# Kernel tuning notes

Hardware: AMD Instinct MI355X
Metric: run time of the kernel (lower is better)

The kernel has to match this reference:

```python
import jax, jax.numpy as jnp
import numpy as np

BS, SEQ, NUM_SKILLS, DIM_S, SIZE_M = 64, 200, 4096, 256, 64

def setup_inputs():
    key = jax.random.key(0)
    ks = jax.random.split(key, 16)
    def n(k, shape, s=0.05):
        return jax.random.normal(k, shape, dtype=jnp.float32) * s
    return {
        "q": jax.random.randint(ks[0], (BS, SEQ), 0, NUM_SKILLS),
        "r": jax.random.randint(ks[1], (BS, SEQ), 0, 2),
        "k_emb": n(ks[2], (NUM_SKILLS, DIM_S)),
        "x_emb": n(ks[3], (2 * NUM_SKILLS + 1, DIM_S)),
        "Mk": n(ks[4], (SIZE_M, DIM_S)),
        "Mv0": n(ks[5], (SIZE_M, DIM_S)),
        "W_a": n(ks[6], (DIM_S, 2 * DIM_S)), "b_a": jnp.zeros((DIM_S,), jnp.float32),
        "W_e": n(ks[7], (DIM_S, DIM_S)), "b_e": jnp.zeros((DIM_S,), jnp.float32),
        "W_add": n(ks[8], (DIM_S, DIM_S)), "b_add": jnp.zeros((DIM_S,), jnp.float32),
        "W_f": n(ks[9], (DIM_S, 2 * DIM_S)), "b_f": jnp.zeros((DIM_S,), jnp.float32),
        "hx": n(ks[10], (1, DIM_S)), "cx": n(ks[11], (1, DIM_S)),
        "W_ih": n(ks[12], (4 * DIM_S, DIM_S)), "b_ih": jnp.zeros((4 * DIM_S,), jnp.float32),
        "W_hh": n(ks[13], (4 * DIM_S, DIM_S)), "b_hh": jnp.zeros((4 * DIM_S,), jnp.float32),
        "W_p": n(ks[14], (1, DIM_S)), "b_p": jnp.zeros((1,), jnp.float32),
    }

def _forward(q, r, k_emb, x_emb, Mk, Mv0, W_a, b_a, W_e, b_e, W_add, b_add,
             W_f, b_f, hx, cx, W_ih, b_ih, W_hh, b_hh, W_p, b_p):
    num_skills = k_emb.shape[0]
    bs = q.shape[0]
    k = k_emb[q]                                    # (bs, seq, d) question key embedding
    v = x_emb[q + num_skills * r]                   # (bs, seq, d) interaction embedding
    # DKVMN addressing against the static key memory Mk (precomputable for all t)
    w = jax.nn.softmax(jnp.einsum('bsd,md->bsm', k, Mk), axis=-1)
    # write control input: a_embed(cat(k, v)), then erase/add head projections
    we = jnp.einsum('bse,de->bsd', jnp.concatenate([k, v], axis=-1), W_a) + b_a
    erase = jax.nn.sigmoid(jnp.einsum('bsd,ed->bse', we, W_e) + b_e)
    add = jnp.tanh(jnp.einsum('bsd,ed->bse', we, W_add) + b_add)
    mem0 = jnp.broadcast_to(Mv0, (bs,) + Mv0.shape)  # (bs, m, d)

    def mem_step(mem, inp):
        wt, et, at = inp                             # (bs,m), (bs,d), (bs,d)
        read = jnp.einsum('bm,bmd->bd', wt, mem)     # weighted read BEFORE write
        ww = wt[:, :, None]
        mem = mem * (1.0 - ww * et[:, None, :]) + ww * at[:, None, :]
        return mem, read

    _, reads = jax.lax.scan(mem_step, mem0,
                            (w.transpose(1, 0, 2), erase.transpose(1, 0, 2), add.transpose(1, 0, 2)))
    reads = reads.transpose(1, 0, 2)                 # (bs, seq, d)
    f = jnp.tanh(jnp.einsum('bse,de->bsd', jnp.concatenate([reads, k], axis=-1), W_f) + b_f)

    def lstm_step(carry, ft):
        h, c = carry
        gates = ft @ W_ih.T + b_ih + h @ W_hh.T + b_hh
        i_g, f_g, g_g, o_g = jnp.split(gates, 4, axis=-1)  # torch LSTMCell gate order
        c = jax.nn.sigmoid(f_g) * c + jax.nn.sigmoid(i_g) * jnp.tanh(g_g)
        h = jax.nn.sigmoid(o_g) * jnp.tanh(c)
        return (h, c), h

    d = hx.shape[1]
    h0 = jnp.broadcast_to(hx, (bs, d))
    c0 = jnp.broadcast_to(cx, (bs, d))
    _, hs = jax.lax.scan(lstm_step, (h0, c0), f.transpose(1, 0, 2))
    hs = hs.transpose(1, 0, 2)                       # (bs, seq, d)
    p = jax.nn.sigmoid(jnp.einsum('bsd,od->bso', hs, W_p) + b_p)[..., 0]
    return p                                         # (bs, seq)

def reference(q, r, k_emb, x_emb, Mk, Mv0, W_a, b_a, W_e, b_e, W_add, b_add,
              W_f, b_f, hx, cx, W_ih, b_ih, W_hh, b_hh, W_p, b_p):
    return _forward(q, r, k_emb, x_emb, Mk, Mv0, W_a, b_a, W_e, b_e, W_add, b_add,
                    W_f, b_f, hx, cx, W_ih, b_ih, W_hh, b_hh, W_p, b_p)
```

## Files before the change

### kernel.cpp

```cpp
#include <hip/hip_runtime.h>
#include <hip/hip_bf16.h>

#define BS 64
#define SEQ 200
#define NSK 4096
#define DS 256
#define SM 64
#define NROWS (BS*SEQ)
#define LBLK 8

typedef __attribute__((ext_vector_type(8))) short bf16x8;
typedef __attribute__((ext_vector_type(4))) float f32x4;

__device__ __forceinline__ float sigf(float x){ return 1.0f/(1.0f+expf(-x)); }
__device__ __forceinline__ float fast_sig(float x){ return 1.0f/(1.0f+__expf(-x)); }
__device__ __forceinline__ float fast_tanh(float x){
  float t = __expf(-2.0f*fabsf(x));
  float r = (1.0f - t)/(1.0f + t);
  return copysignf(r, x);
}
__device__ __forceinline__ short f2bf(float x){
  unsigned int u = __float_as_uint(x);
  unsigned int r = (u + 0x7fffu + ((u >> 16) & 1u)) >> 16;
  return (short)r;
}
__device__ __forceinline__ float bf2f(unsigned short s){
  return __uint_as_float(((unsigned int)s) << 16);
}

__global__ __launch_bounds__(256) void k_gather_attn(
    const int* __restrict__ q, const int* __restrict__ r,
    const float* __restrict__ k_emb, const float* __restrict__ x_emb,
    const float* __restrict__ Mk,
    float* __restrict__ X2, float* __restrict__ vbuf, float* __restrict__ wbuf)
{
  __shared__ float ks[4][DS];
  const int tid = threadIdx.x;
  const int wv = tid >> 6, ln = tid & 63;
  const int row = blockIdx.x * 4 + wv;
  const int b = row / SEQ, s = row % SEQ;
  const int qi = q[b*SEQ + s];
  const int ri = r[b*SEQ + s];
  const float4* kr = (const float4*)(k_emb + (size_t)qi * DS);
  const float4* vr = (const float4*)(x_emb + ((size_t)qi + (size_t)NSK * ri) * DS);
  float4 kv = kr[ln];
  float4 vv = vr[ln];
  ((float4*)(X2 + (size_t)row*512 + DS))[ln] = kv;
  ((float4*)(vbuf + (size_t)row*DS))[ln] = vv;
  *((float4*)&ks[wv][ln*4]) = kv;
  __syncthreads();
  const float4* mkr = (const float4*)(Mk + (size_t)ln * DS);
  float a0=0.f,a1=0.f,a2=0.f,a3=0.f;
  #pragma unroll 8
  for (int d4=0; d4<DS/4; d4++){
    float4 m4 = mkr[d4];
    float4 k4 = *((const float4*)&ks[wv][d4*4]);
    a0 += m4.x*k4.x; a1 += m4.y*k4.y; a2 += m4.z*k4.z; a3 += m4.w*k4.w;
  }
  float lg = (a0+a1)+(a2+a3);
  float mx = lg;
  #pragma unroll
  for (int off=32; off; off>>=1) mx = fmaxf(mx, __shfl_xor(mx, off));
  float ex = expf(lg - mx);
  float sm = ex;
  #pragma unroll
  for (int off=32; off; off>>=1) sm += __shfl_xor(sm, off);
  wbuf[(size_t)row*SM + ln] = ex / sm;
}

template<int ACT>
__global__ __launch_bounds__(256) void k_gemm_bf16(
    const float* __restrict__ A0, int lda0, int K0,
    const float* __restrict__ A1, int lda1, int K1,
    const float* __restrict__ W, const float* __restrict__ bias,
    const float* __restrict__ bias2,
    float* __restrict__ C, int N)
{
  const int K = K0 + K1;
  __shared__ __align__(16) char As[64*80];
  __shared__ __align__(16) char Bs[64*80];
  const int tid = threadIdx.x;
  const int l = tid & 63, w = tid >> 6;
  const int m0 = blockIdx.x * 64, n0 = blockIdx.y * 64;
  const int mh = w >> 1, nh = w & 1;
  const int srow = tid >> 2, sseg = tid & 3;

  f32x4 acc[2][2];
  #pragma unroll
  for (int i=0;i<2;i++)
    #pragma unroll
    for (int j=0;j<2;j++) acc[i][j] = (f32x4){0.f,0.f,0.f,0.f};

  for (int k0=0; k0<K; k0+=32){
    const int kk = k0 + sseg*8;
    const float* ap;
    if (kk < K0) ap = A0 + (size_t)(m0+srow)*lda0 + kk;
    else         ap = A1 + (size_t)(m0+srow)*lda1 + (kk - K0);
    float4 a1 = *(const float4*)ap;
    float4 a2 = *(const float4*)(ap+4);
    bf16x8 av;
    av[0]=f2bf(a1.x); av[1]=f2bf(a1.y); av[2]=f2bf(a1.z); av[3]=f2bf(a1.w);
    av[4]=f2bf(a2.x); av[5]=f2bf(a2.y); av[6]=f2bf(a2.z); av[7]=f2bf(a2.w);
    *(bf16x8*)(As + srow*80 + ((sseg ^ (srow&3))*16)) = av;
    const float* wp = W + (size_t)(n0+srow)*K + kk;
    float4 b1 = *(const float4*)wp;
    float4 b2 = *(const float4*)(wp+4);
    bf16x8 bv;
    bv[0]=f2bf(b1.x); bv[1]=f2bf(b1.y); bv[2]=f2bf(b1.z); bv[3]=f2bf(b1.w);
    bv[4]=f2bf(b2.x); bv[5]=f2bf(b2.y); bv[6]=f2bf(b2.z); bv[7]=f2bf(b2.w);
    *(bf16x8*)(Bs + srow*80 + ((sseg ^ (srow&3))*16)) = bv;
    __syncthreads();
    bf16x8 af[2], bf[2];
    #pragma unroll
    for (int mi=0; mi<2; mi++){
      const int row = mh*32 + mi*16 + (l&15);
      af[mi] = *(const bf16x8*)(As + row*80 + (((l>>4) ^ (row&3))*16));
    }
    #pragma unroll
    for (int ni=0; ni<2; ni++){
      const int row = nh*32 + ni*16 + (l&15);
      bf[ni] = *(const bf16x8*)(Bs + row*80 + (((l>>4) ^ (row&3))*16));
    }
    #pragma unroll
    for (int mi=0; mi<2; mi++)
      #pragma unroll
      for (int ni=0; ni<2; ni++)
        acc[mi][ni] = __builtin_amdgcn_mfma_f32_16x16x32_bf16(af[mi], bf[ni], acc[mi][ni], 0,0,0);
    __syncthreads();
  }
  #pragma unroll
  for (int mi=0; mi<2; mi++){
    #pragma unroll
    for (int ni=0; ni<2; ni++){
      const int n = n0 + nh*32 + ni*16 + (l&15);
      float bsum = bias[n] + (bias2 ? bias2[n] : 0.f);
      #pragma unroll
      for (int j=0;j<4;j++){
        const int m = m0 + mh*32 + mi*16 + (l>>4)*4 + j;
        float v = acc[mi][ni][j] + bsum;
        if (ACT==1) v = sigf(v);
        else if (ACT==2) v = tanhf(v);
        C[(size_t)m*N + n] = v;
      }
    }
  }
}

__global__ __launch_bounds__(256) void k_scan(
    const float* __restrict__ wbuf, const float* __restrict__ ebuf,
    const float* __restrict__ abuf, const float* __restrict__ Mv0,
    float* __restrict__ X2)
{
  const int b = blockIdx.x;
  const int d = threadIdx.x;
  __shared__ float ws[SM];
  float mem[SM];
  #pragma unroll
  for (int m=0;m<SM;m++) mem[m] = Mv0[m*DS + d];
  for (int t=0;t<SEQ;t++){
    const size_t row = (size_t)b*SEQ + t;
    if (d < SM) ws[d] = wbuf[row*SM + d];
    const float e = ebuf[row*DS + d];
    const float a = abuf[row*DS + d];
    __syncthreads();
    float r0=0.f,r1=0.f,r2=0.f,r3=0.f;
    #pragma unroll
    for (int m=0;m<SM;m+=4){
      float w0=ws[m], w1=ws[m+1], w2=ws[m+2], w3=ws[m+3];
      r0 += w0*mem[m];   mem[m]   += w0*fmaf(-e, mem[m],   a);
      r1 += w1*mem[m+1]; mem[m+1] += w1*fmaf(-e, mem[m+1], a);
      r2 += w2*mem[m+2]; mem[m+2] += w2*fmaf(-e, mem[m+2], a);
      r3 += w3*mem[m+3]; mem[m+3] += w3*fmaf(-e, mem[m+3], a);
    }
    X2[row*512 + d] = (r0+r1)+(r2+r3);
    __syncthreads();
  }
}

__global__ __launch_bounds__(512, 2) void k_lstm2(
    const float* __restrict__ gin, const float* __restrict__ W_hh,
    const float* __restrict__ hx, const float* __restrict__ cx,
    short* __restrict__ hhist, unsigned long long* __restrict__ xbuf)
{
  const int bb = blockIdx.x;
  const int p  = bb >> 1;
  const int ro = bb & 1;
  const int tid = threadIdx.x;
  const int l   = tid & 63;
  const int w   = tid >> 6;

  __shared__ short hsm[2][16*256];

  bf16x8 wfr[4][8];
  {
    const int col  = l & 15;
    const int krow = (l >> 4) * 8;
    #pragma unroll
    for (int gt=0; gt<4; gt++){
      const int G = gt*256 + ro*128 + w*16 + col;
      const float* wrow = W_hh + (size_t)G*256;
      #pragma unroll
      for (int kt=0; kt<8; kt++){
        const int k0 = kt*32 + krow;
        float4 wa = *(const float4*)(wrow + k0);
        float4 wb = *(const float4*)(wrow + k0 + 4);
        bf16x8 f;
        f[0]=f2bf(wa.x); f[1]=f2bf(wa.y); f[2]=f2bf(wa.z); f[3]=f2bf(wa.w);
        f[4]=f2bf(wb.x); f[5]=f2bf(wb.y); f[6]=f2bf(wb.z); f[7]=f2bf(wb.w);
        wfr[gt][kt] = f;
      }
    }
  }

  const int dhalf = w*16 + (l & 15);
  const int gdim  = ro*128 + dhalf;
  float c_[4];
  {
    float c0 = cx[gdim];
    #pragma unroll
    for (int r=0;r<4;r++) c_[r] = c0;
  }

  if (tid < 256){
    const int row = tid >> 4, seg = tid & 15;
    #pragma unroll
    for (int u=0; u<2; u++){
      const int kb = seg*32 + u*16;
      const int d0 = kb >> 1;
      float4 ha = *(const float4*)(hx + d0);
      float4 hb = *(const float4*)(hx + d0 + 4);
      bf16x8 v;
      v[0]=f2bf(ha.x); v[1]=f2bf(ha.y); v[2]=f2bf(ha.z); v[3]=f2bf(ha.w);
      v[4]=f2bf(hb.x); v[5]=f2bf(hb.y); v[6]=f2bf(hb.z); v[7]=f2bf(hb.w);
      *(bf16x8*)((char*)hsm[0] + row*512 + (kb ^ ((row&7)<<4))) = v;
    }
  }

  float gpre[16];
  #pragma unroll
  for (int gt=0; gt<4; gt++)
    #pragma unroll
    for (int r=0; r<4; r++){
      const int b = p*16 + (l>>4)*4 + r;
      gpre[gt*4+r] = gin[((size_t)(b*SEQ))*1024 + gt*256 + gdim];
    }

  unsigned long long* myslots = xbuf + (size_t)(p*2 + ro)*1024;
  unsigned long long* pslots  = xbuf + (size_t)(p*2 + (1-ro))*1024;

  for (int t=0; t<SEQ; t++){
    __syncthreads();
    const int cur = t & 1;

    f32x4 acc[4];
    #pragma unroll
    for (int gt=0; gt<4; gt++) acc[gt] = (f32x4){0.f,0.f,0.f,0.f};
    const int r0 = l & 15;
    #pragma unroll
    for (int kt=0; kt<8; kt++){
      const int kbyte = kt*64 + (l>>4)*16;
      bf16x8 a = *(const bf16x8*)((const char*)hsm[cur] + r0*512 + (kbyte ^ ((r0&7)<<4)));
      #pragma unroll
      for (int gt=0; gt<4; gt++)
        acc[gt] = __builtin_amdgcn_mfma_f32_16x16x32_bf16(a, wfr[gt][kt], acc[gt], 0,0,0);
    }

    const unsigned int tag = (unsigned int)(t + 1);
    #pragma unroll
    for (int r=0; r<4; r++){
      const int bat = (l>>4)*4 + r;
      const int b = p*16 + bat;
      float iv = gpre[0*4+r] + acc[0][r];
      float fv = gpre[1*4+r] + acc[1][r];
      float gv = gpre[2*4+r] + acc[2][r];
      float ov = gpre[3*4+r] + acc[3][r];
      float cc = fast_sig(fv)*c_[r] + fast_sig(iv)*fast_tanh(gv);
      c_[r] = cc;
      float h = fast_sig(ov)*fast_tanh(cc);
      unsigned short hb = (unsigned short)f2bf(h);
      hhist[((size_t)(b*SEQ + t))*256 + gdim] = (short)hb;
      *(short*)((char*)hsm[cur^1] + bat*512 + ((gdim*2) ^ ((bat&7)<<4))) = (short)hb;
      unsigned short nb = (unsigned short)__shfl_xor((int)hb, 1);
      if ((l & 1) == 0){
        unsigned long long v = ((unsigned long long)hb << 48)
                             | ((unsigned long long)nb << 32)
                             | (unsigned long long)tag;
        __hip_atomic_store(&myslots[bat*64 + (dhalf>>1)], v,
                           __ATOMIC_RELAXED, __HIP_MEMORY_SCOPE_AGENT);
      }
    }

    if (t == SEQ-1) break;

    #pragma unroll
    for (int gt=0; gt<4; gt++)
      #pragma unroll
      for (int r=0; r<4; r++){
        const int b = p*16 + (l>>4)*4 + r;
        gpre[gt*4+r] = gin[((size_t)(b*SEQ + t+1))*1024 + gt*256 + gdim];
      }

    {
      const int s0 = tid*2, s1 = tid*2 + 1;
      unsigned long long v0=0, v1=0;
      bool ok0=false, ok1=false;
      while (true){
        if (!ok0){ v0 = __hip_atomic_load(&pslots[s0], __ATOMIC_RELAXED, __HIP_MEMORY_SCOPE_AGENT);
                   ok0 = ((unsigned int)v0 == tag); }
        if (!ok1){ v1 = __hip_atomic_load(&pslots[s1], __ATOMIC_RELAXED, __HIP_MEMORY_SCOPE_AGENT);
                   ok1 = ((unsigned int)v1 == tag); }
        if (ok0 && ok1) break;
        __builtin_amdgcn_s_sleep(1);
      }
      #pragma unroll
      for (int u=0; u<2; u++){
        unsigned long long v = u ? v1 : v0;
        const int sid = u ? s1 : s0;
        const int bat = sid >> 6;
        const int dp  = sid & 63;
        const int dpart = (1-ro)*128 + dp*2;
        unsigned int wv = (unsigned int)((v >> 48) & 0xffffu)
                        | (((unsigned int)(v >> 32) & 0xffffu) << 16);
        *(unsigned int*)((char*)hsm[cur^1] + bat*512 + ((dpart*2) ^ ((bat&7)<<4))) = wv;
      }
    }
  }
}

__global__ __launch_bounds__(256) void k_pout(
    const short* __restrict__ hhist, const float* __restrict__ W_p,
    const float* __restrict__ b_p, float* __restrict__ out)
{
  const int tid = threadIdx.x;
  const int row = blockIdx.x*4 + (tid>>6);
  const int ln = tid & 63;
  ushort4 hv = ((const ushort4*)(hhist + (size_t)row*256))[ln];
  float4 wp = ((const float4*)W_p)[ln];
  float s = bf2f(hv.x)*wp.x + bf2f(hv.y)*wp.y + bf2f(hv.z)*wp.z + bf2f(hv.w)*wp.w;
  #pragma unroll
  for (int off=32; off; off>>=1) s += __shfl_xor(s, off);
  if (ln == 0) out[row] = sigf(s + b_p[0]);
}

extern "C" void kernel_launch(void* const* d_in, const int* in_sizes, int n_in,
                              void* d_out, int out_size, void* d_ws, size_t ws_size,
                              hipStream_t stream)
{
  const int*   q     = (const int*)d_in[0];
  const int*   r     = (const int*)d_in[1];
  const float* k_emb = (const float*)d_in[2];
  const float* x_emb = (const float*)d_in[3];
  const float* Mk    = (const float*)d_in[4];
  const float* Mv0   = (const float*)d_in[5];
  const float* W_a   = (const float*)d_in[6];
  const float* b_a   = (const float*)d_in[7];
  const float* W_e   = (const float*)d_in[8];
  const float* b_e   = (const float*)d_in[9];
  const float* W_add = (const float*)d_in[10];
  const float* b_add = (const float*)d_in[11];
  const float* W_f   = (const float*)d_in[12];
  const float* b_f   = (const float*)d_in[13];
  const float* hx    = (const float*)d_in[14];
  const float* cx    = (const float*)d_in[15];
  const float* W_ih  = (const float*)d_in[16];
  const float* b_ih  = (const float*)d_in[17];
  const float* W_hh  = (const float*)d_in[18];
  const float* b_hh  = (const float*)d_in[19];
  const float* W_p   = (const float*)d_in[20];
  const float* b_p   = (const float*)d_in[21];
  float* out = (float*)d_out;

  float* ws    = (float*)d_ws;
  float* vbuf  = ws;
  float* webuf = vbuf  + (size_t)NROWS*DS;
  float* ebuf  = webuf + (size_t)NROWS*DS;
  float* abuf  = ebuf  + (size_t)NROWS*DS;
  float* gin   = vbuf;
  float* X2    = abuf  + (size_t)NROWS*DS;
  float* wbuf  = X2    + (size_t)NROWS*512;
  float* fbuf  = wbuf  + (size_t)NROWS*SM;
  short* hhist = (short*)fbuf;
  unsigned long long* xbuf = (unsigned long long*)(fbuf + (size_t)NROWS*DS);

  k_gather_attn<<<NROWS/4, 256, 0, stream>>>(q, r, k_emb, x_emb, Mk, X2, vbuf, wbuf);
  k_gemm_bf16<0><<<dim3(NROWS/64, 4), 256, 0, stream>>>(X2+DS, 512, DS, vbuf, DS, DS, W_a, b_a, nullptr, webuf, DS);
  k_gemm_bf16<1><<<dim3(NROWS/64, 4), 256, 0, stream>>>(webuf, DS, DS, webuf, DS, 0, W_e,   b_e,   nullptr, ebuf, DS);
  k_gemm_bf16<2><<<dim3(NROWS/64, 4), 256, 0, stream>>>(webuf, DS, DS, webuf, DS, 0, W_add, b_add, nullptr, abuf, DS);
  k_scan<<<BS, DS, 0, stream>>>(wbuf, ebuf, abuf, Mv0, X2);
  k_gemm_bf16<2><<<dim3(NROWS/64, 4), 256, 0, stream>>>(X2, 512, DS, X2+DS, 512, DS, W_f, b_f, nullptr, fbuf, DS);
  k_gemm_bf16<0><<<dim3(NROWS/64, 16), 256, 0, stream>>>(fbuf, DS, DS, fbuf, DS, 0, W_ih, b_ih, b_hh, gin, 1024);
  {
    const float* gin_c = gin;
    void* args[] = { (void*)&gin_c, (void*)&W_hh, (void*)&hx, (void*)&cx,
                     (void*)&hhist, (void*)&xbuf };
    hipLaunchCooperativeKernel((void*)k_lstm2, dim3(LBLK), dim3(512), args, 0, stream);
  }
  k_pout<<<NROWS/4, 256, 0, stream>>>(hhist, W_p, b_p, out);
}
```

Before: 1.029 ms.

## Store intermediates in bf16, fuse erase/add GEMMs, interleave LSTM gate inputs

The write-embedding, f, and LSTM input-gate buffers are now stored as bf16 instead of fp32, which halves their global traffic and removes a conversion step in the consuming GEMMs. The erase and add projections run in one kernel that loads the shared A tile once. The gate pre-activations are written interleaved per dimension, so each LSTM step fetches all four gates with a single 64-bit load on the serial critical path. The cost is extra rounding of the gate inputs to bf16 and hardcoded workspace byte offsets.

```diff
diff --git a/kernel.cpp b/kernel.cpp
--- a/kernel.cpp
+++ b/kernel.cpp
@@ -11,6 +11,7 @@
 
 typedef __attribute__((ext_vector_type(8))) short bf16x8;
 typedef __attribute__((ext_vector_type(4))) float f32x4;
+typedef unsigned long long u64;
 
 __device__ __forceinline__ float sigf(float x){ return 1.0f/(1.0f+expf(-x)); }
 __device__ __forceinline__ float fast_sig(float x){ return 1.0f/(1.0f+__expf(-x)); }
@@ -68,13 +69,13 @@
   wbuf[(size_t)row*SM + ln] = ex / sm;
 }
 
-template<int ACT>
-__global__ __launch_bounds__(256) void k_gemm_bf16(
-    const float* __restrict__ A0, int lda0, int K0,
-    const float* __restrict__ A1, int lda1, int K1,
+template<int ACT, int ABF, int OUT>
+__global__ __launch_bounds__(256) void k_gemm2(
+    const void* __restrict__ A0, int lda0, int K0,
+    const void* __restrict__ A1, int lda1, int K1,
     const float* __restrict__ W, const float* __restrict__ bias,
     const float* __restrict__ bias2,
-    float* __restrict__ C, int N)
+    void* __restrict__ C, int N)
 {
   const int K = K0 + K1;
   __shared__ __align__(16) char As[64*80];
@@ -93,14 +94,19 @@
 
   for (int k0=0; k0<K; k0+=32){
     const int kk = k0 + sseg*8;
-    const float* ap;
-    if (kk < K0) ap = A0 + (size_t)(m0+srow)*lda0 + kk;
-    else         ap = A1 + (size_t)(m0+srow)*lda1 + (kk - K0);
-    float4 a1 = *(const float4*)ap;
-    float4 a2 = *(const float4*)(ap+4);
     bf16x8 av;
-    av[0]=f2bf(a1.x); av[1]=f2bf(a1.y); av[2]=f2bf(a1.z); av[3]=f2bf(a1.w);
-    av[4]=f2bf(a2.x); av[5]=f2bf(a2.y); av[6]=f2bf(a2.z); av[7]=f2bf(a2.w);
+    if (ABF){
+      const ushort* ap = (kk < K0) ? (const ushort*)A0 + (size_t)(m0+srow)*lda0 + kk
+                                   : (const ushort*)A1 + (size_t)(m0+srow)*lda1 + (kk-K0);
+      av = *(const bf16x8*)ap;
+    } else {
+      const float* ap = (kk < K0) ? (const float*)A0 + (size_t)(m0+srow)*lda0 + kk
+                                  : (const float*)A1 + (size_t)(m0+srow)*lda1 + (kk-K0);
+      float4 a1 = *(const float4*)ap;
+      float4 a2 = *(const float4*)(ap+4);
+      av[0]=f2bf(a1.x); av[1]=f2bf(a1.y); av[2]=f2bf(a1.z); av[3]=f2bf(a1.w);
+      av[4]=f2bf(a2.x); av[5]=f2bf(a2.y); av[6]=f2bf(a2.z); av[7]=f2bf(a2.w);
+    }
     *(bf16x8*)(As + srow*80 + ((sseg ^ (srow&3))*16)) = av;
     const float* wp = W + (size_t)(n0+srow)*K + kk;
     float4 b1 = *(const float4*)wp;
@@ -140,7 +146,88 @@
         float v = acc[mi][ni][j] + bsum;
         if (ACT==1) v = sigf(v);
         else if (ACT==2) v = tanhf(v);
-        C[(size_t)m*N + n] = v;
+        if (OUT==0)      ((float*)C)[(size_t)m*N + n] = v;
+        else if (OUT==1) ((ushort*)C)[(size_t)m*N + n] = (ushort)f2bf(v);
+        else             ((ushort*)C)[(size_t)m*N + ((n&255)*4 + (n>>8))] = (ushort)f2bf(v);
+      }
+    }
+  }
+}
+
+__global__ __launch_bounds__(256) void k_gemm_ea(
+    const ushort* __restrict__ A, const float* __restrict__ W_e,
+    const float* __restrict__ b_e, const float* __restrict__ W_add,
+    const float* __restrict__ b_add,
+    float* __restrict__ ebuf, float* __restrict__ abuf)
+{
+  __shared__ __align__(16) char As[64*80];
+  __shared__ __align__(16) char Bse[64*80];
+  __shared__ __align__(16) char Bsa[64*80];
+  const int tid = threadIdx.x;
+  const int l = tid & 63, w = tid >> 6;
+  const int m0 = blockIdx.x * 64, n0 = blockIdx.y * 64;
+  const int mh = w >> 1, nh = w & 1;
+  const int srow = tid >> 2, sseg = tid & 3;
+
+  f32x4 acce[2][2], acca[2][2];
+  #pragma unroll
+  for (int i=0;i<2;i++)
+    #pragma unroll
+    for (int j=0;j<2;j++){ acce[i][j]=(f32x4){0.f,0.f,0.f,0.f}; acca[i][j]=(f32x4){0.f,0.f,0.f,0.f}; }
+
+  for (int k0=0; k0<DS; k0+=32){
+    const int kk = k0 + sseg*8;
+    bf16x8 av = *(const bf16x8*)(A + (size_t)(m0+srow)*DS + kk);
+    *(bf16x8*)(As + srow*80 + ((sseg ^ (srow&3))*16)) = av;
+    {
+      const float* wp = W_e + (size_t)(n0+srow)*DS + kk;
+      float4 b1 = *(const float4*)wp; float4 b2 = *(const float4*)(wp+4);
+      bf16x8 bv;
+      bv[0]=f2bf(b1.x); bv[1]=f2bf(b1.y); bv[2]=f2bf(b1.z); bv[3]=f2bf(b1.w);
+      bv[4]=f2bf(b2.x); bv[5]=f2bf(b2.y); bv[6]=f2bf(b2.z); bv[7]=f2bf(b2.w);
+      *(bf16x8*)(Bse + srow*80 + ((sseg ^ (srow&3))*16)) = bv;
+    }
+    {
+      const float* wp = W_add + (size_t)(n0+srow)*DS + kk;
+      float4 b1 = *(const float4*)wp; float4 b2 = *(const float4*)(wp+4);
+      bf16x8 bv;
+      bv[0]=f2bf(b1.x); bv[1]=f2bf(b1.y); bv[2]=f2bf(b1.z); bv[3]=f2bf(b1.w);
+      bv[4]=f2bf(b2.x); bv[5]=f2bf(b2.y); bv[6]=f2bf(b2.z); bv[7]=f2bf(b2.w);
+      *(bf16x8*)(Bsa + srow*80 + ((sseg ^ (srow&3))*16)) = bv;
+    }
+    __syncthreads();
+    bf16x8 af[2], bfe[2], bfa[2];
+    #pragma unroll
+    for (int mi=0; mi<2; mi++){
+      const int row = mh*32 + mi*16 + (l&15);
+      af[mi] = *(const bf16x8*)(As + row*80 + (((l>>4) ^ (row&3))*16));
+    }
+    #pragma unroll
+    for (int ni=0; ni<2; ni++){
+      const int row = nh*32 + ni*16 + (l&15);
+      bfe[ni] = *(const bf16x8*)(Bse + row*80 + (((l>>4) ^ (row&3))*16));
+      bfa[ni] = *(const bf16x8*)(Bsa + row*80 + (((l>>4) ^ (row&3))*16));
+    }
+    #pragma unroll
+    for (int mi=0; mi<2; mi++)
+      #pragma unroll
+      for (int ni=0; ni<2; ni++){
+        acce[mi][ni] = __builtin_amdgcn_mfma_f32_16x16x32_bf16(af[mi], bfe[ni], acce[mi][ni], 0,0,0);
+        acca[mi][ni] = __builtin_amdgcn_mfma_f32_16x16x32_bf16(af[mi], bfa[ni], acca[mi][ni], 0,0,0);
+      }
+    __syncthreads();
+  }
+  #pragma unroll
+  for (int mi=0; mi<2; mi++){
+    #pragma unroll
+    for (int ni=0; ni<2; ni++){
+      const int n = n0 + nh*32 + ni*16 + (l&15);
+      const float be = b_e[n], ba = b_add[n];
+      #pragma unroll
+      for (int j=0;j<4;j++){
+        const int m = m0 + mh*32 + mi*16 + (l>>4)*4 + j;
+        ebuf[(size_t)m*DS + n] = sigf(acce[mi][ni][j] + be);
+        abuf[(size_t)m*DS + n] = tanhf(acca[mi][ni][j] + ba);
       }
     }
   }
@@ -178,7 +265,7 @@
 }
 
 __global__ __launch_bounds__(512, 2) void k_lstm2(
-    const float* __restrict__ gin, const float* __restrict__ W_hh,
+    const ushort* __restrict__ gin2, const float* __restrict__ W_hh,
     const float* __restrict__ hx, const float* __restrict__ cx,
     short* __restrict__ hhist, unsigned long long* __restrict__ xbuf)
 {
@@ -236,14 +323,12 @@
     }
   }
 
-  float gpre[16];
-  #pragma unroll
-  for (int gt=0; gt<4; gt++)
-    #pragma unroll
-    for (int r=0; r<4; r++){
-      const int b = p*16 + (l>>4)*4 + r;
-      gpre[gt*4+r] = gin[((size_t)(b*SEQ))*1024 + gt*256 + gdim];
-    }
+  u64 gpre[4];
+  #pragma unroll
+  for (int r=0; r<4; r++){
+    const int b = p*16 + (l>>4)*4 + r;
+    gpre[r] = *(const u64*)(gin2 + ((size_t)(b*SEQ))*1024 + gdim*4);
+  }
 
   unsigned long long* myslots = xbuf + (size_t)(p*2 + ro)*1024;
   unsigned long long* pslots  = xbuf + (size_t)(p*2 + (1-ro))*1024;
@@ -270,11 +355,12 @@
     for (int r=0; r<4; r++){
       const int bat = (l>>4)*4 + r;
       const int b = p*16 + bat;
-      float iv = gpre[0*4+r] + acc[0][r];
-      float fv = gpre[1*4+r] + acc[1][r];
-      float gv = gpre[2*4+r] + acc[2][r];
-      float ov = gpre[3*4+r] + acc[3][r];
-      float cc = fast_sig(fv)*c_[r] + fast_sig(iv)*fast_tanh(gv);
+      const u64 gv = gpre[r];
+      float iv = acc[0][r] + bf2f((unsigned short)(gv       & 0xffffu));
+      float fv = acc[1][r] + bf2f((unsigned short)((gv>>16) & 0xffffu));
+      float gg = acc[2][r] + bf2f((unsigned short)((gv>>32) & 0xffffu));
+      float ov = acc[3][r] + bf2f((unsigned short)((gv>>48) & 0xffffu));
+      float cc = fast_sig(fv)*c_[r] + fast_sig(iv)*fast_tanh(gg);
       c_[r] = cc;
       float h = fast_sig(ov)*fast_tanh(cc);
       unsigned short hb = (unsigned short)f2bf(h);
@@ -293,12 +379,10 @@
     if (t == SEQ-1) break;
 
     #pragma unroll
-    for (int gt=0; gt<4; gt++)
-      #pragma unroll
-      for (int r=0; r<4; r++){
-        const int b = p*16 + (l>>4)*4 + r;
-        gpre[gt*4+r] = gin[((size_t)(b*SEQ + t+1))*1024 + gt*256 + gdim];
-      }
+    for (int r=0; r<4; r++){
+      const int b = p*16 + (l>>4)*4 + r;
+      gpre[r] = *(const u64*)(gin2 + ((size_t)(b*SEQ + t+1))*1024 + gdim*4);
+    }
 
     {
       const int s0 = tid*2, s1 = tid*2 + 1;
@@ -370,27 +454,26 @@
   const float* b_p   = (const float*)d_in[21];
   float* out = (float*)d_out;
 
-  float* ws    = (float*)d_ws;
-  float* vbuf  = ws;
-  float* webuf = vbuf  + (size_t)NROWS*DS;
-  float* ebuf  = webuf + (size_t)NROWS*DS;
-  float* abuf  = ebuf  + (size_t)NROWS*DS;
-  float* gin   = vbuf;
-  float* X2    = abuf  + (size_t)NROWS*DS;
-  float* wbuf  = X2    + (size_t)NROWS*512;
-  float* fbuf  = wbuf  + (size_t)NROWS*SM;
-  short* hhist = (short*)fbuf;
-  unsigned long long* xbuf = (unsigned long long*)(fbuf + (size_t)NROWS*DS);
+  char* base = (char*)d_ws;
+  float*  vbuf  = (float*)(base);
+  ushort* webuf = (ushort*)(base + 13107200);
+  float*  ebuf  = (float*)(base + 19660800);
+  float*  abuf  = (float*)(base + 32768000);
+  float*  X2    = (float*)(base + 45875200);
+  float*  wbuf  = (float*)(base + 72089600);
+  ushort* fbuf  = (ushort*)(base + 75366400);
+  ushort* gin2  = (ushort*)(base);
+  short*  hhist = (short*)fbuf;
+  unsigned long long* xbuf = (unsigned long long*)(base + 81920000);
 
   k_gather_attn<<<NROWS/4, 256, 0, stream>>>(q, r, k_emb, x_emb, Mk, X2, vbuf, wbuf);
-  k_gemm_bf16<0><<<dim3(NROWS/64, 4), 256, 0, stream>>>(X2+DS, 512, DS, vbuf, DS, DS, W_a, b_a, nullptr, webuf, DS);
-  k_gemm_bf16<1><<<dim3(NROWS/64, 4), 256, 0, stream>>>(webuf, DS, DS, webuf, DS, 0, W_e,   b_e,   nullptr, ebuf, DS);
-  k_gemm_bf16<2><<<dim3(NROWS/64, 4), 256, 0, stream>>>(webuf, DS, DS, webuf, DS, 0, W_add, b_add, nullptr, abuf, DS);
+  k_gemm2<0,0,1><<<dim3(NROWS/64, 4), 256, 0, stream>>>(X2+DS, 512, DS, vbuf, DS, DS, W_a, b_a, nullptr, webuf, DS);
+  k_gemm_ea<<<dim3(NROWS/64, 4), 256, 0, stream>>>(webuf, W_e, b_e, W_add, b_add, ebuf, abuf);
   k_scan<<<BS, DS, 0, stream>>>(wbuf, ebuf, abuf, Mv0, X2);
-  k_gemm_bf16<2><<<dim3(NROWS/64, 4), 256, 0, stream>>>(X2, 512, DS, X2+DS, 512, DS, W_f, b_f, nullptr, fbuf, DS);
-  k_gemm_bf16<0><<<dim3(NROWS/64, 16), 256, 0, stream>>>(fbuf, DS, DS, fbuf, DS, 0, W_ih, b_ih, b_hh, gin, 1024);
+  k_gemm2<2,0,1><<<dim3(NROWS/64, 4), 256, 0, stream>>>(X2, 512, DS, X2+DS, 512, DS, W_f, b_f, nullptr, fbuf, DS);
+  k_gemm2<0,1,2><<<dim3(NROWS/64, 16), 256, 0, stream>>>(fbuf, DS, DS, fbuf, DS, 0, W_ih, b_ih, b_hh, gin2, 1024);
   {
-    const float* gin_c = gin;
+    const ushort* gin_c = gin2;
     void* args[] = { (void*)&gin_c, (void*)&W_hh, (void*)&hx, (void*)&cx,
                      (void*)&hhist, (void*)&xbuf };
     hipLaunchCooperativeKernel((void*)k_lstm2, dim3(LBLK), dim3(512), args, 0, stream);
```

After: 1.039 ms. Within noise of the previous version (+1.0%).
